# Optimization experiments

Measured on AMD Instinct MI355X. Metric: run time of the kernel, lower is better.

## Reference

```python
import jax, jax.numpy as jnp
import numpy as np

EPS = 1e-3  # keras LayerNormalization default epsilon

def setup_inputs() -> dict:
    key = jax.random.key(0)
    k1, k2 = jax.random.split(key)
    B, N, D, M = 16, 4096, 768, 8
    x = jax.random.normal(k1, (B, N, D), dtype=jnp.float32)
    queries = jax.random.normal(k2, (M, D), dtype=jnp.float32)
    gamma = jnp.ones((D,), dtype=jnp.float32)
    beta = jnp.zeros((D,), dtype=jnp.float32)
    return {"x": x, "queries": queries, "gamma": gamma, "beta": beta}

def reference(x, queries, gamma, beta):
    D = x.shape[-1]
    scale = D ** -0.5
    # LayerNorm over last dim (keras default: epsilon=1e-3, learned gamma/beta)
    mu = jnp.mean(x, axis=-1, keepdims=True)
    var = jnp.mean(jnp.square(x - mu), axis=-1, keepdims=True)
    xn = (x - mu) * jax.lax.rsqrt(var + EPS) * gamma + beta  # [B, N, D]
    # sim = queries @ (x^T * scale) -> [B, M, N]
    sim = jnp.einsum('md,bnd->bmn', queries, xn) * scale
    attn = jax.nn.softmax(sim, axis=-1)
    # out = attn @ x_normed -> [B, M, D]
    return jnp.einsum('bmn,bnd->bmd', attn, xn)
```

## Files before the change

### kernel.cpp

```cpp
#include <hip/hip_runtime.h>
#include <hip/hip_bf16.h>


#define B_ 16
#define N_ 4096
#define D_ 768
#define M_ 8
#define EPS_ 1e-3f
#define SCALE_ 0.03608439182435161f

#define SIM_OFF   0
#define MEAN_OFF  524288
#define RSTD_OFF  589824
#define SMAX_OFF  655360
#define SINV_OFF  655488

__global__ __launch_bounds__(256) void k_ln_sim(
    const float* __restrict__ x,
    const float* __restrict__ q,
    const float* __restrict__ gm,
    const float* __restrict__ bt,
    float* __restrict__ sim, float* __restrict__ meanb, float* __restrict__ rstdb)
{
    __shared__ __align__(16) float qg_s[8][768];
    __shared__ float qgs_s[8], qb_s[8];

    const int lane = threadIdx.x & 63;
    const int wv   = threadIdx.x >> 6;
    const int gw   = blockIdx.x * 4 + wv;
    const int total_waves = gridDim.x * 4;

    {
        const int m0 = wv * 2, m1 = m0 + 1;
        float qgs0 = 0.f, qb0 = 0.f, qgs1 = 0.f, qb1 = 0.f;
#pragma unroll
        for (int i = 0; i < 3; i++) {
            const int c4 = (lane + i * 64) * 4;
            const float4 gv = *(const float4*)(gm + c4);
            const float4 bv = *(const float4*)(bt + c4);
            const float4 q0 = *(const float4*)(q + m0 * D_ + c4);
            const float4 q1 = *(const float4*)(q + m1 * D_ + c4);
            float4 g0, g1;
            g0.x = q0.x * gv.x; g0.y = q0.y * gv.y; g0.z = q0.z * gv.z; g0.w = q0.w * gv.w;
            g1.x = q1.x * gv.x; g1.y = q1.y * gv.y; g1.z = q1.z * gv.z; g1.w = q1.w * gv.w;
            *(float4*)&qg_s[m0][c4] = g0;
            *(float4*)&qg_s[m1][c4] = g1;
            qgs0 += g0.x + g0.y + g0.z + g0.w;
            qgs1 += g1.x + g1.y + g1.z + g1.w;
            qb0  += q0.x * bv.x + q0.y * bv.y + q0.z * bv.z + q0.w * bv.w;
            qb1  += q1.x * bv.x + q1.y * bv.y + q1.z * bv.z + q1.w * bv.w;
        }
#pragma unroll
        for (int mask = 32; mask; mask >>= 1) {
            qgs0 += __shfl_xor(qgs0, mask, 64);
            qgs1 += __shfl_xor(qgs1, mask, 64);
            qb0  += __shfl_xor(qb0,  mask, 64);
            qb1  += __shfl_xor(qb1,  mask, 64);
        }
        if (lane == 0) {
            qgs_s[m0] = qgs0; qgs_s[m1] = qgs1;
            qb_s[m0]  = qb0;  qb_s[m1]  = qb1;
        }
    }
    __syncthreads();

    const int mo = lane >> 3;
    const float qgs_sel = qgs_s[mo];
    const float qbs     = SCALE_ * qb_s[mo];

    const bool hi32 = (lane & 32) != 0;
    const bool hi16 = (lane & 16) != 0;
    const bool hi8  = (lane & 8)  != 0;

    for (int row = gw; row < B_ * N_; row += total_waves) {
        const float* xr = x + (size_t)row * D_;
        float v[12];
#pragma unroll
        for (int i = 0; i < 3; i++) {
            float4 p = *(const float4*)(xr + (lane + i * 64) * 4);
            v[i * 4 + 0] = p.x; v[i * 4 + 1] = p.y;
            v[i * 4 + 2] = p.z; v[i * 4 + 3] = p.w;
        }
        float s = 0.f, s2 = 0.f;
#pragma unroll
        for (int k = 0; k < 12; k++) { s += v[k]; s2 += v[k] * v[k]; }

        float acc[8];
#pragma unroll
        for (int m = 0; m < 8; m++) acc[m] = 0.f;
#pragma unroll
        for (int i = 0; i < 3; i++) {
            const int c4 = (lane + i * 64) * 4;
#pragma unroll
            for (int m = 0; m < 8; m++) {
                const float4 qv = *(const float4*)&qg_s[m][c4];
                acc[m] = fmaf(qv.x, v[i * 4 + 0], acc[m]);
                acc[m] = fmaf(qv.y, v[i * 4 + 1], acc[m]);
                acc[m] = fmaf(qv.z, v[i * 4 + 2], acc[m]);
                acc[m] = fmaf(qv.w, v[i * 4 + 3], acc[m]);
            }
        }

#pragma unroll
        for (int mask = 32; mask; mask >>= 1) {
            s  += __shfl_xor(s,  mask, 64);
            s2 += __shfl_xor(s2, mask, 64);
        }
        const float mean = s * (1.0f / 768.0f);
        float var = s2 * (1.0f / 768.0f) - mean * mean;
        var = fmaxf(var, 0.0f);
        const float rstd = rsqrtf(var + EPS_);

        float a0 = hi32 ? acc[4] : acc[0], sA0 = hi32 ? acc[0] : acc[4];
        float a1 = hi32 ? acc[5] : acc[1], sA1 = hi32 ? acc[1] : acc[5];
        float a2 = hi32 ? acc[6] : acc[2], sA2 = hi32 ? acc[2] : acc[6];
        float a3 = hi32 ? acc[7] : acc[3], sA3 = hi32 ? acc[3] : acc[7];
        a0 += __shfl_xor(sA0, 32, 64);
        a1 += __shfl_xor(sA1, 32, 64);
        a2 += __shfl_xor(sA2, 32, 64);
        a3 += __shfl_xor(sA3, 32, 64);
        float b0 = hi16 ? a2 : a0, sB0 = hi16 ? a0 : a2;
        float b1 = hi16 ? a3 : a1, sB1 = hi16 ? a1 : a3;
        b0 += __shfl_xor(sB0, 16, 64);
        b1 += __shfl_xor(sB1, 16, 64);
        float c0 = hi8 ? b1 : b0, sC0 = hi8 ? b0 : b1;
        c0 += __shfl_xor(sC0, 8, 64);
        c0 += __shfl_xor(c0, 4, 64);
        c0 += __shfl_xor(c0, 2, 64);
        c0 += __shfl_xor(c0, 1, 64);

        const int b = row >> 12, n = row & (N_ - 1);
        if (lane == 0) {
            meanb[row] = mean;
            rstdb[row] = rstd;
        }
        if ((lane & 7) == 0) {
            sim[(size_t)((b * 8 + mo) << 12) + n] =
                fmaf(rstd * SCALE_, c0 - mean * qgs_sel, qbs);
        }
    }
}

__global__ __launch_bounds__(256) void k_stats(
    const float* __restrict__ sim,
    const float* __restrict__ meanb,
    const float* __restrict__ rstdb,
    const float* __restrict__ gm,
    const float* __restrict__ bt,
    float* __restrict__ smax, float* __restrict__ sinv,
    float* __restrict__ out)
{
    const int bm = blockIdx.x;
    const int b  = bm >> 3;
    const float* p  = sim   + ((size_t)bm << 12);
    const float* mu = meanb + ((size_t)b  << 12);
    const float* rs = rstdb + ((size_t)b  << 12);
    const int t = threadIdx.x;
    const int lane = t & 63, wave = t >> 6;
    __shared__ float red[8];

    float v[16];
    float mx = -3.4e38f;
#pragma unroll
    for (int i = 0; i < 16; i++) { v[i] = p[t + i * 256]; mx = fmaxf(mx, v[i]); }
#pragma unroll
    for (int mask = 32; mask; mask >>= 1) mx = fmaxf(mx, __shfl_xor(mx, mask, 64));
    if (lane == 0) red[wave] = mx;
    __syncthreads();
    mx = fmaxf(fmaxf(red[0], red[1]), fmaxf(red[2], red[3]));
    __syncthreads();

    float s = 0.f, smu = 0.f;
#pragma unroll
    for (int i = 0; i < 16; i++) {
        const int n = t + i * 256;
        const float e = __expf(v[i] - mx);
        s += e;
        smu = fmaf(e, rs[n] * mu[n], smu);
    }
#pragma unroll
    for (int mask = 32; mask; mask >>= 1) {
        s   += __shfl_xor(s,   mask, 64);
        smu += __shfl_xor(smu, mask, 64);
    }
    if (lane == 0) { red[wave] = s; red[wave + 4] = smu; }
    __syncthreads();
    s   = red[0] + red[1] + red[2] + red[3];
    smu = red[4] + red[5] + red[6] + red[7];
    const float inv = 1.0f / s;
    const float wmu = smu * inv;
    if (t == 0) { smax[bm] = mx; sinv[bm] = inv; }

    float* o = out + (size_t)bm * D_;
#pragma unroll
    for (int k = 0; k < 3; k++) {
        const int d = t + k * 256;
        o[d] = fmaf(-gm[d], wmu, bt[d]);
    }
}

__global__ __launch_bounds__(256) void k_out(
    const float* __restrict__ x,
    const float* __restrict__ gm,
    const float* __restrict__ sim,
    const float* __restrict__ rstdb,
    const float* __restrict__ smax,
    const float* __restrict__ sinv,
    float* __restrict__ out)
{
    __shared__ __align__(16) float w_s[8 * 256];

    const int b  = blockIdx.x;
    const int dc = blockIdx.y;
    const int nc = blockIdx.z;
    const int t  = threadIdx.x;
    const int n0 = nc << 8;
    const int d  = (dc << 8) + t;

    const float rs_t = rstdb[((size_t)b << 12) + n0 + t];
#pragma unroll
    for (int m = 0; m < 8; m++) {
        const int bm = (b << 3) + m;
        const float v = sim[((size_t)bm << 12) + n0 + t];
        w_s[(m << 8) + t] = __expf(v - smax[bm]) * sinv[bm] * rs_t;
    }
    __syncthreads();

    float acc[8];
#pragma unroll
    for (int m = 0; m < 8; m++) acc[m] = 0.f;

    const float* xp = x + ((size_t)(b * N_ + n0)) * D_ + d;
#pragma unroll 2
    for (int nn = 0; nn < 256; nn += 4) {
        const float x0 = xp[(size_t)(nn + 0) * D_];
        const float x1 = xp[(size_t)(nn + 1) * D_];
        const float x2 = xp[(size_t)(nn + 2) * D_];
        const float x3 = xp[(size_t)(nn + 3) * D_];
#pragma unroll
        for (int m = 0; m < 8; m++) {
            const float4 wv = *(const float4*)&w_s[(m << 8) + nn];
            acc[m] = fmaf(wv.x, x0, acc[m]);
            acc[m] = fmaf(wv.y, x1, acc[m]);
            acc[m] = fmaf(wv.z, x2, acc[m]);
            acc[m] = fmaf(wv.w, x3, acc[m]);
        }
    }

    const float g = gm[d];
#pragma unroll
    for (int mm = 0; mm < 8; mm++) {
        const int m = (mm + nc) & 7;
        atomicAdd(out + (size_t)((b << 3) + m) * D_ + d, g * acc[m]);
    }
}

extern "C" void kernel_launch(void* const* d_in, const int* in_sizes, int n_in,
                              void* d_out, int out_size, void* d_ws, size_t ws_size,
                              hipStream_t stream)
{
    const float* x  = (const float*)d_in[0];
    const float* q  = (const float*)d_in[1];
    const float* gm = (const float*)d_in[2];
    const float* bt = (const float*)d_in[3];
    float* out = (float*)d_out;

    float* ws    = (float*)d_ws;
    float* sim   = ws + SIM_OFF;
    float* meanb = ws + MEAN_OFF;
    float* rstdb = ws + RSTD_OFF;
    float* smax  = ws + SMAX_OFF;
    float* sinv  = ws + SINV_OFF;

    k_ln_sim<<<1536, 256, 0, stream>>>(x, q, gm, bt, sim, meanb, rstdb);
    k_stats<<<B_ * M_, 256, 0, stream>>>(sim, meanb, rstdb, gm, bt, smax, sinv, out);
    k_out<<<dim3(16, 3, 16), 256, 0, stream>>>(x, gm, sim, rstdb, smax, sinv, out);
}
```

Before: 316.9 us.

## Process two rows per wave in LN-sim, precompute softmax weights, split k_out finer

The LN+sim kernel now has each wave handle two rows per iteration with a fixed grid of 1024 blocks, so every shared-memory read of the query vector serves two rows. The stats kernel now writes the final softmax weights (already multiplied by rstd) to a workspace buffer. k_out reads those weights straight from global memory instead of recomputing exp in shared memory, and uses half-size n chunks with twice as many blocks. The trade-offs are an extra global write/read of the weight buffer, more register pressure, and twice the atomic adds into the output.

```diff
diff --git a/kernel.cpp b/kernel.cpp
--- a/kernel.cpp
+++ b/kernel.cpp
@@ -12,8 +12,7 @@
 #define SIM_OFF   0
 #define MEAN_OFF  524288
 #define RSTD_OFF  589824
-#define SMAX_OFF  655360
-#define SINV_OFF  655488
+#define WBUF_OFF  655360
 
 __global__ __launch_bounds__(256) void k_ln_sim(
     const float* __restrict__ x,
@@ -27,8 +26,6 @@
 
     const int lane = threadIdx.x & 63;
     const int wv   = threadIdx.x >> 6;
-    const int gw   = blockIdx.x * 4 + wv;
-    const int total_waves = gridDim.x * 4;
 
     {
         const int m0 = wv * 2, m1 = m0 + 1;
@@ -72,71 +69,99 @@
     const bool hi16 = (lane & 16) != 0;
     const bool hi8  = (lane & 8)  != 0;
 
-    for (int row = gw; row < B_ * N_; row += total_waves) {
-        const float* xr = x + (size_t)row * D_;
-        float v[12];
-#pragma unroll
-        for (int i = 0; i < 3; i++) {
-            float4 p = *(const float4*)(xr + (lane + i * 64) * 4);
-            v[i * 4 + 0] = p.x; v[i * 4 + 1] = p.y;
-            v[i * 4 + 2] = p.z; v[i * 4 + 3] = p.w;
-        }
-        float s = 0.f, s2 = 0.f;
-#pragma unroll
-        for (int k = 0; k < 12; k++) { s += v[k]; s2 += v[k] * v[k]; }
-
-        float acc[8];
-#pragma unroll
-        for (int m = 0; m < 8; m++) acc[m] = 0.f;
+    const int gw = blockIdx.x * 4 + wv;
+
+#pragma unroll 1
+    for (int it = 0; it < 8; ++it) {
+        const int pr   = gw + (it << 12);
+        const int row0 = pr * 2;
+        const float* xr0 = x + (size_t)row0 * D_;
+
+        float v0[12], v1[12];
 #pragma unroll
         for (int i = 0; i < 3; i++) {
             const int c4 = (lane + i * 64) * 4;
+            const float4 p0 = *(const float4*)(xr0 + c4);
+            const float4 p1 = *(const float4*)(xr0 + D_ + c4);
+            v0[i * 4 + 0] = p0.x; v0[i * 4 + 1] = p0.y; v0[i * 4 + 2] = p0.z; v0[i * 4 + 3] = p0.w;
+            v1[i * 4 + 0] = p1.x; v1[i * 4 + 1] = p1.y; v1[i * 4 + 2] = p1.z; v1[i * 4 + 3] = p1.w;
+        }
+
+        float s0 = 0.f, s20 = 0.f, s1 = 0.f, s21 = 0.f;
+#pragma unroll
+        for (int k = 0; k < 12; k++) {
+            s0 += v0[k]; s20 += v0[k] * v0[k];
+            s1 += v1[k]; s21 += v1[k] * v1[k];
+        }
+
+        float acc0[8], acc1[8];
+#pragma unroll
+        for (int m = 0; m < 8; m++) { acc0[m] = 0.f; acc1[m] = 0.f; }
+#pragma unroll
+        for (int i = 0; i < 3; i++) {
+            const int c4 = (lane + i * 64) * 4;
 #pragma unroll
             for (int m = 0; m < 8; m++) {
                 const float4 qv = *(const float4*)&qg_s[m][c4];
-                acc[m] = fmaf(qv.x, v[i * 4 + 0], acc[m]);
-                acc[m] = fmaf(qv.y, v[i * 4 + 1], acc[m]);
-                acc[m] = fmaf(qv.z, v[i * 4 + 2], acc[m]);
-                acc[m] = fmaf(qv.w, v[i * 4 + 3], acc[m]);
+                acc0[m] = fmaf(qv.x, v0[i * 4 + 0], acc0[m]);
+                acc0[m] = fmaf(qv.y, v0[i * 4 + 1], acc0[m]);
+                acc0[m] = fmaf(qv.z, v0[i * 4 + 2], acc0[m]);
+                acc0[m] = fmaf(qv.w, v0[i * 4 + 3], acc0[m]);
+                acc1[m] = fmaf(qv.x, v1[i * 4 + 0], acc1[m]);
+                acc1[m] = fmaf(qv.y, v1[i * 4 + 1], acc1[m]);
+                acc1[m] = fmaf(qv.z, v1[i * 4 + 2], acc1[m]);
+                acc1[m] = fmaf(qv.w, v1[i * 4 + 3], acc1[m]);
             }
         }
 
 #pragma unroll
         for (int mask = 32; mask; mask >>= 1) {
-            s  += __shfl_xor(s,  mask, 64);
-            s2 += __shfl_xor(s2, mask, 64);
-        }
-        const float mean = s * (1.0f / 768.0f);
-        float var = s2 * (1.0f / 768.0f) - mean * mean;
-        var = fmaxf(var, 0.0f);
-        const float rstd = rsqrtf(var + EPS_);
-
-        float a0 = hi32 ? acc[4] : acc[0], sA0 = hi32 ? acc[0] : acc[4];
-        float a1 = hi32 ? acc[5] : acc[1], sA1 = hi32 ? acc[1] : acc[5];
-        float a2 = hi32 ? acc[6] : acc[2], sA2 = hi32 ? acc[2] : acc[6];
-        float a3 = hi32 ? acc[7] : acc[3], sA3 = hi32 ? acc[3] : acc[7];
-        a0 += __shfl_xor(sA0, 32, 64);
-        a1 += __shfl_xor(sA1, 32, 64);
-        a2 += __shfl_xor(sA2, 32, 64);
-        a3 += __shfl_xor(sA3, 32, 64);
+            s0  += __shfl_xor(s0,  mask, 64);
+            s1  += __shfl_xor(s1,  mask, 64);
+            s20 += __shfl_xor(s20, mask, 64);
+            s21 += __shfl_xor(s21, mask, 64);
+        }
+        const float mean0 = s0 * (1.0f / 768.0f);
+        const float mean1 = s1 * (1.0f / 768.0f);
+        float var0 = fmaxf(s20 * (1.0f / 768.0f) - mean0 * mean0, 0.0f);
+        float var1 = fmaxf(s21 * (1.0f / 768.0f) - mean1 * mean1, 0.0f);
+        const float rstd0 = rsqrtf(var0 + EPS_);
+        const float rstd1 = rsqrtf(var1 + EPS_);
+
+        float a0 = hi32 ? acc0[4] : acc0[0], sA0 = hi32 ? acc0[0] : acc0[4];
+        float a1 = hi32 ? acc0[5] : acc0[1], sA1 = hi32 ? acc0[1] : acc0[5];
+        float a2 = hi32 ? acc0[6] : acc0[2], sA2 = hi32 ? acc0[2] : acc0[6];
+        float a3 = hi32 ? acc0[7] : acc0[3], sA3 = hi32 ? acc0[3] : acc0[7];
+        float e0 = hi32 ? acc1[4] : acc1[0], sE0 = hi32 ? acc1[0] : acc1[4];
+        float e1 = hi32 ? acc1[5] : acc1[1], sE1 = hi32 ? acc1[1] : acc1[5];
+        float e2 = hi32 ? acc1[6] : acc1[2], sE2 = hi32 ? acc1[2] : acc1[6];
+        float e3 = hi32 ? acc1[7] : acc1[3], sE3 = hi32 ? acc1[3] : acc1[7];
+        a0 += __shfl_xor(sA0, 32, 64);  e0 += __shfl_xor(sE0, 32, 64);
+        a1 += __shfl_xor(sA1, 32, 64);  e1 += __shfl_xor(sE1, 32, 64);
+        a2 += __shfl_xor(sA2, 32, 64);  e2 += __shfl_xor(sE2, 32, 64);
+        a3 += __shfl_xor(sA3, 32, 64);  e3 += __shfl_xor(sE3, 32, 64);
         float b0 = hi16 ? a2 : a0, sB0 = hi16 ? a0 : a2;
         float b1 = hi16 ? a3 : a1, sB1 = hi16 ? a1 : a3;
-        b0 += __shfl_xor(sB0, 16, 64);
-        b1 += __shfl_xor(sB1, 16, 64);
+        float f0 = hi16 ? e2 : e0, sF0 = hi16 ? e0 : e2;
+        float f1 = hi16 ? e3 : e1, sF1 = hi16 ? e1 : e3;
+        b0 += __shfl_xor(sB0, 16, 64);  f0 += __shfl_xor(sF0, 16, 64);
+        b1 += __shfl_xor(sB1, 16, 64);  f1 += __shfl_xor(sF1, 16, 64);
         float c0 = hi8 ? b1 : b0, sC0 = hi8 ? b0 : b1;
-        c0 += __shfl_xor(sC0, 8, 64);
-        c0 += __shfl_xor(c0, 4, 64);
-        c0 += __shfl_xor(c0, 2, 64);
-        c0 += __shfl_xor(c0, 1, 64);
-
-        const int b = row >> 12, n = row & (N_ - 1);
+        float g0 = hi8 ? f1 : f0, sG0 = hi8 ? f0 : f1;
+        c0 += __shfl_xor(sC0, 8, 64);   g0 += __shfl_xor(sG0, 8, 64);
+        c0 += __shfl_xor(c0, 4, 64);    g0 += __shfl_xor(g0, 4, 64);
+        c0 += __shfl_xor(c0, 2, 64);    g0 += __shfl_xor(g0, 2, 64);
+        c0 += __shfl_xor(c0, 1, 64);    g0 += __shfl_xor(g0, 1, 64);
+
+        const int b = row0 >> 12, n0 = row0 & (N_ - 1);
         if (lane == 0) {
-            meanb[row] = mean;
-            rstdb[row] = rstd;
+            meanb[row0]     = mean0;  rstdb[row0]     = rstd0;
+            meanb[row0 + 1] = mean1;  rstdb[row0 + 1] = rstd1;
         }
         if ((lane & 7) == 0) {
-            sim[(size_t)((b * 8 + mo) << 12) + n] =
-                fmaf(rstd * SCALE_, c0 - mean * qgs_sel, qbs);
+            float* sp = sim + (size_t)((b * 8 + mo) << 12) + n0;
+            sp[0] = fmaf(rstd0 * SCALE_, c0 - mean0 * qgs_sel, qbs);
+            sp[1] = fmaf(rstd1 * SCALE_, g0 - mean1 * qgs_sel, qbs);
         }
     }
 }
@@ -147,7 +172,7 @@
     const float* __restrict__ rstdb,
     const float* __restrict__ gm,
     const float* __restrict__ bt,
-    float* __restrict__ smax, float* __restrict__ sinv,
+    float* __restrict__ wbuf,
     float* __restrict__ out)
 {
     const int bm = blockIdx.x;
@@ -170,13 +195,16 @@
     mx = fmaxf(fmaxf(red[0], red[1]), fmaxf(red[2], red[3]));
     __syncthreads();
 
+    float rsv[16];
     float s = 0.f, smu = 0.f;
 #pragma unroll
     for (int i = 0; i < 16; i++) {
         const int n = t + i * 256;
         const float e = __expf(v[i] - mx);
+        rsv[i] = rs[n];
         s += e;
-        smu = fmaf(e, rs[n] * mu[n], smu);
+        smu = fmaf(e, rsv[i] * mu[n], smu);
+        v[i] = e;
     }
 #pragma unroll
     for (int mask = 32; mask; mask >>= 1) {
@@ -189,7 +217,11 @@
     smu = red[4] + red[5] + red[6] + red[7];
     const float inv = 1.0f / s;
     const float wmu = smu * inv;
-    if (t == 0) { smax[bm] = mx; sinv[bm] = inv; }
+
+    float* wrow = wbuf + ((size_t)bm << 12);
+#pragma unroll
+    for (int i = 0; i < 16; i++)
+        wrow[t + i * 256] = v[i] * inv * rsv[i];
 
     float* o = out + (size_t)bm * D_;
 #pragma unroll
@@ -202,48 +234,36 @@
 __global__ __launch_bounds__(256) void k_out(
     const float* __restrict__ x,
     const float* __restrict__ gm,
-    const float* __restrict__ sim,
-    const float* __restrict__ rstdb,
-    const float* __restrict__ smax,
-    const float* __restrict__ sinv,
+    const float* __restrict__ wbuf,
     float* __restrict__ out)
 {
-    __shared__ __align__(16) float w_s[8 * 256];
-
     const int b  = blockIdx.x;
     const int dc = blockIdx.y;
     const int nc = blockIdx.z;
     const int t  = threadIdx.x;
-    const int n0 = nc << 8;
+    const int n0 = nc << 7;
     const int d  = (dc << 8) + t;
 
-    const float rs_t = rstdb[((size_t)b << 12) + n0 + t];
-#pragma unroll
-    for (int m = 0; m < 8; m++) {
-        const int bm = (b << 3) + m;
-        const float v = sim[((size_t)bm << 12) + n0 + t];
-        w_s[(m << 8) + t] = __expf(v - smax[bm]) * sinv[bm] * rs_t;
-    }
-    __syncthreads();
+    const float* wr = wbuf + ((size_t)(b << 3) << 12) + n0;
+    const float* xp = x + ((size_t)(b * N_ + n0)) * D_ + d;
 
     float acc[8];
 #pragma unroll
     for (int m = 0; m < 8; m++) acc[m] = 0.f;
 
-    const float* xp = x + ((size_t)(b * N_ + n0)) * D_ + d;
 #pragma unroll 2
-    for (int nn = 0; nn < 256; nn += 4) {
+    for (int nn = 0; nn < 128; nn += 4) {
         const float x0 = xp[(size_t)(nn + 0) * D_];
         const float x1 = xp[(size_t)(nn + 1) * D_];
         const float x2 = xp[(size_t)(nn + 2) * D_];
         const float x3 = xp[(size_t)(nn + 3) * D_];
 #pragma unroll
         for (int m = 0; m < 8; m++) {
-            const float4 wv = *(const float4*)&w_s[(m << 8) + nn];
-            acc[m] = fmaf(wv.x, x0, acc[m]);
-            acc[m] = fmaf(wv.y, x1, acc[m]);
-            acc[m] = fmaf(wv.z, x2, acc[m]);
-            acc[m] = fmaf(wv.w, x3, acc[m]);
+            const float4 wq = *(const float4*)(wr + ((size_t)m << 12) + nn);
+            acc[m] = fmaf(wq.x, x0, acc[m]);
+            acc[m] = fmaf(wq.y, x1, acc[m]);
+            acc[m] = fmaf(wq.z, x2, acc[m]);
+            acc[m] = fmaf(wq.w, x3, acc[m]);
         }
     }
 
@@ -269,10 +289,9 @@
     float* sim   = ws + SIM_OFF;
     float* meanb = ws + MEAN_OFF;
     float* rstdb = ws + RSTD_OFF;
-    float* smax  = ws + SMAX_OFF;
-    float* sinv  = ws + SINV_OFF;
-
-    k_ln_sim<<<1536, 256, 0, stream>>>(x, q, gm, bt, sim, meanb, rstdb);
-    k_stats<<<B_ * M_, 256, 0, stream>>>(sim, meanb, rstdb, gm, bt, smax, sinv, out);
-    k_out<<<dim3(16, 3, 16), 256, 0, stream>>>(x, gm, sim, rstdb, smax, sinv, out);
-}
+    float* wbuf  = ws + WBUF_OFF;
+
+    k_ln_sim<<<1024, 256, 0, stream>>>(x, q, gm, bt, sim, meanb, rstdb);
+    k_stats<<<B_ * M_, 256, 0, stream>>>(sim, meanb, rstdb, gm, bt, wbuf, out);
+    k_out<<<dim3(16, 3, 32), 256, 0, stream>>>(x, gm, wbuf, out);
+}
```

Result: slower. 332.1 us (+4.8%).
